# Kernel optimization log

Hardware: AMD Instinct MI355X
Metric: run time of the kernel (lower is better)

Reference implementation:

```python
import jax, jax.numpy as jnp
import numpy as np

B, S, D, H = 16, 4096, 768, 12  # batch, seqlen, dim, num_heads
KS = 9  # res_kernel_size


def setup_inputs() -> dict:
    key = jax.random.key(0)
    ks = jax.random.split(key, 6)
    x = jax.random.normal(ks[0], (B, S, D), dtype=jnp.float32)
    w_qkv = jax.random.normal(ks[1], (3 * D, D), dtype=jnp.float32) * 0.02
    b_qkv = jax.random.normal(ks[2], (3 * D,), dtype=jnp.float32) * 0.02
    w_proj = jax.random.normal(ks[3], (D, D), dtype=jnp.float32) * 0.02
    b_proj = jax.random.normal(ks[4], (D,), dtype=jnp.float32) * 0.02
    # depthwise conv over (seq, head_dim) spatial dims: kernel (KS, 1), groups=H
    w_dconv = jax.random.normal(ks[5], (H, 1, KS, 1), dtype=jnp.float32) * 0.1
    return {"x": x, "w_qkv": w_qkv, "b_qkv": b_qkv,
            "w_proj": w_proj, "b_proj": b_proj, "w_dconv": w_dconv}


def reference(x, w_qkv, b_qkv, w_proj, b_proj, w_dconv):
    Bz, Sz, Dz = x.shape
    Hh = w_dconv.shape[0]
    d = Dz // Hh  # head_dim
    # qkv projection: [B,S,3D] -> [3,B,H,S,d]  (rearrange 's (n h d) -> n h s d')
    qkv = jnp.einsum('bsd,ed->bse', x, w_qkv) + b_qkv
    qkv = qkv.reshape(Bz, Sz, 3, Hh, d).transpose(2, 0, 3, 1, 4)
    q, k, v = qkv[0], qkv[1], qkv[2]  # each [B,H,S,d]
    # L2-normalize q, k along head dim
    q = q / jnp.linalg.norm(q, axis=-1, keepdims=True)
    k = k / jnp.linalg.norm(k, axis=-1, keepdims=True)
    # depthwise conv on v: NCHW = [B, H, S, d], kernel (KS,1), pad (KS//2, 0)
    pad = w_dconv.shape[2] // 2
    dconv_v = jax.lax.conv_general_dilated(
        v, w_dconv, window_strides=(1, 1),
        padding=((pad, pad), (0, 0)), feature_group_count=Hh)
    # linear angular attention: kv = k^T v  ([B,H,d,d]), then q @ kv
    kv = jnp.einsum('bhsd,bhse->bhde', k, v)
    out = 0.5 * v + (1.0 / jnp.pi) * jnp.einsum('bhsd,bhde->bhse', q, kv)
    out = out / jnp.linalg.norm(out, axis=-1, keepdims=True)
    out = out + dconv_v
    # 'h s d -> s (h d)' (with batch): [B,H,S,d] -> [B,S,H*d]
    out = out.transpose(0, 2, 1, 3).reshape(Bz, Sz, Dz)
    return jnp.einsum('bsd,ed->bse', out, w_proj) + b_proj
```

## Files before the change

### kernel.cpp

```cpp
#include <hip/hip_runtime.h>
#include <hip/hip_bf16.h>

#define DEV __device__ __forceinline__

typedef __attribute__((ext_vector_type(8))) short bf16x8;
typedef __attribute__((ext_vector_type(4))) float f32x4;

DEV unsigned short bfbits(float x) {
    __hip_bfloat16 b = __float2bfloat16(x);
    return __builtin_bit_cast(unsigned short, b);
}
DEV float b2f(unsigned short u) {
    __hip_bfloat16 b = __builtin_bit_cast(__hip_bfloat16, u);
    return __bfloat162float(b);
}

DEV void gl2lds16(const void* g, void* l) {
    __builtin_amdgcn_global_load_lds(
        (const __attribute__((address_space(1))) void*)g,
        (__attribute__((address_space(3))) void*)l,
        16, 0, 0);
}

DEV void stC(float* p, float v) { *p = v; }
DEV void stC(__hip_bfloat16* p, float v) { *p = __float2bfloat16(v); }

__global__ __launch_bounds__(256) void cvt_bf16(const float* __restrict__ in,
                                                unsigned short* __restrict__ out, int n) {
    int i = (blockIdx.x * 256 + threadIdx.x) * 4;
    if (i >= n) return;
    float4 f = *(const float4*)(in + i);
    ushort4 u;
    u.x = bfbits(f.x); u.y = bfbits(f.y); u.z = bfbits(f.z); u.w = bfbits(f.w);
    *(ushort4*)(out + i) = u;
}

template <typename OutT>
__global__ __launch_bounds__(256) void gemm_bt(const __hip_bfloat16* __restrict__ A,
                                               const __hip_bfloat16* __restrict__ B,
                                               const float* __restrict__ bias,
                                               OutT* __restrict__ C,
                                               int M, int N, int K) {
    __shared__ __align__(16) unsigned short As[128 * 32];
    __shared__ __align__(16) unsigned short Bs[128 * 32];
    const int t = threadIdx.x;
    const int wave = t >> 6, lane = t & 63;
    const int quad = lane >> 4, l16 = lane & 15;
    const int m0 = blockIdx.y * 128, n0 = blockIdx.x * 128;
    const int wm = (wave & 1) * 64, wn = (wave >> 1) * 64;
    const int r0 = t >> 2;
    const int c0 = (t & 3) * 8;
    const unsigned short* Au = (const unsigned short*)A;
    const unsigned short* Bu = (const unsigned short*)B;

    f32x4 acc[4][4] = {};
    for (int k0 = 0; k0 < K; k0 += 32) {
        gl2lds16(Au + (size_t)(m0 + r0) * K + k0 + c0,      As + t * 8);
        gl2lds16(Au + (size_t)(m0 + 64 + r0) * K + k0 + c0, As + 2048 + t * 8);
        gl2lds16(Bu + (size_t)(n0 + r0) * K + k0 + c0,      Bs + t * 8);
        gl2lds16(Bu + (size_t)(n0 + 64 + r0) * K + k0 + c0, Bs + 2048 + t * 8);
        __syncthreads();
        bf16x8 af[4], bfr[4];
#pragma unroll
        for (int i = 0; i < 4; i++)
            af[i] = *(const bf16x8*)&As[(wm + i * 16 + l16) * 32 + quad * 8];
#pragma unroll
        for (int j = 0; j < 4; j++)
            bfr[j] = *(const bf16x8*)&Bs[(wn + j * 16 + l16) * 32 + quad * 8];
#pragma unroll
        for (int i = 0; i < 4; i++)
#pragma unroll
            for (int j = 0; j < 4; j++)
                acc[i][j] = __builtin_amdgcn_mfma_f32_16x16x32_bf16(af[i], bfr[j], acc[i][j], 0, 0, 0);
        __syncthreads();
    }
#pragma unroll
    for (int i = 0; i < 4; i++) {
#pragma unroll
        for (int j = 0; j < 4; j++) {
            int col = n0 + wn + j * 16 + l16;
            float bv = bias[col];
#pragma unroll
            for (int r = 0; r < 4; r++) {
                int row = m0 + wm + i * 16 + quad * 4 + r;
                stC(C + (size_t)row * N + col, acc[i][j][r] + bv);
            }
        }
    }
}

__global__ __launch_bounds__(256) void gemm_qkv(const __hip_bfloat16* __restrict__ A,
                                                const __hip_bfloat16* __restrict__ B,
                                                const float* __restrict__ bias,
                                                unsigned short* __restrict__ qhat,
                                                unsigned short* __restrict__ khat,
                                                unsigned short* __restrict__ varr) {
    const int K = 768, NN = 2304;
    __shared__ __align__(16) unsigned short As[128 * 32];
    __shared__ __align__(16) unsigned short Bs[128 * 32];
    const int t = threadIdx.x;
    const int wave = t >> 6, lane = t & 63;
    const int quad = lane >> 4, l16 = lane & 15;
    const int m0 = blockIdx.y * 128, n0 = blockIdx.x * 128;
    const int wm = (wave & 1) * 64, wn = (wave >> 1) * 64;
    const int r0 = t >> 2;
    const int c0 = (t & 3) * 8;
    const unsigned short* Au = (const unsigned short*)A;
    const unsigned short* Bu = (const unsigned short*)B;

    f32x4 acc[4][4] = {};
    for (int k0 = 0; k0 < K; k0 += 32) {
        gl2lds16(Au + (size_t)(m0 + r0) * K + k0 + c0,      As + t * 8);
        gl2lds16(Au + (size_t)(m0 + 64 + r0) * K + k0 + c0, As + 2048 + t * 8);
        gl2lds16(Bu + (size_t)(n0 + r0) * K + k0 + c0,      Bs + t * 8);
        gl2lds16(Bu + (size_t)(n0 + 64 + r0) * K + k0 + c0, Bs + 2048 + t * 8);
        __syncthreads();
        bf16x8 af[4], bfr[4];
#pragma unroll
        for (int i = 0; i < 4; i++)
            af[i] = *(const bf16x8*)&As[(wm + i * 16 + l16) * 32 + quad * 8];
#pragma unroll
        for (int j = 0; j < 4; j++)
            bfr[j] = *(const bf16x8*)&Bs[(wn + j * 16 + l16) * 32 + quad * 8];
#pragma unroll
        for (int i = 0; i < 4; i++)
#pragma unroll
            for (int j = 0; j < 4; j++)
                acc[i][j] = __builtin_amdgcn_mfma_f32_16x16x32_bf16(af[i], bfr[j], acc[i][j], 0, 0, 0);
        __syncthreads();
    }

    const int colbase = n0 + wn;
    const int sec = colbase / 768;
    const int cin = colbase - sec * 768;
    const int h = cin >> 6;
    const int b = m0 >> 12;
    unsigned short* dst = (sec == 0) ? qhat : (sec == 1) ? khat : varr;
    float bv[4];
#pragma unroll
    for (int j = 0; j < 4; j++) bv[j] = bias[colbase + j * 16 + l16];

    const size_t headbase = (size_t)(b * 12 + h) * 4096;
#pragma unroll
    for (int i = 0; i < 4; i++) {
        float o[4][4];
#pragma unroll
        for (int j = 0; j < 4; j++)
#pragma unroll
            for (int r = 0; r < 4; r++) o[j][r] = acc[i][j][r] + bv[j];
        if (sec < 2) {
#pragma unroll
            for (int r = 0; r < 4; r++) {
                float ss = o[0][r]*o[0][r] + o[1][r]*o[1][r] + o[2][r]*o[2][r] + o[3][r]*o[3][r];
                ss += __shfl_xor(ss, 1, 64);
                ss += __shfl_xor(ss, 2, 64);
                ss += __shfl_xor(ss, 4, 64);
                ss += __shfl_xor(ss, 8, 64);
                float sc = rsqrtf(ss);
#pragma unroll
                for (int j = 0; j < 4; j++) o[j][r] *= sc;
            }
        }
#pragma unroll
        for (int j = 0; j < 4; j++)
#pragma unroll
            for (int r = 0; r < 4; r++) {
                int s = (m0 + wm + i * 16 + quad * 4 + r) & 4095;
                dst[(headbase + s) * 64 + j * 16 + l16] = bfbits(o[j][r]);
            }
    }
}

__global__ __launch_bounds__(256) void kv_kernel(const unsigned short* __restrict__ khat,
                                                 const unsigned short* __restrict__ varr,
                                                 float* __restrict__ kvpart) {
    const int bh = blockIdx.x >> 2, chunk = blockIdx.x & 3;
    const int t = threadIdx.x, wave = t >> 6, lane = t & 63;
    __shared__ __align__(16) float kt[64 * 64];
    __shared__ __align__(16) float vt[64 * 64];
    const int e0 = (lane >> 3) * 8, f0 = (lane & 7) * 8;
    float acc[8][8] = {};

    for (int tile = 0; tile < 16; tile++) {
        int sbase = chunk * 1024 + tile * 64;
        __syncthreads();
#pragma unroll
        for (int i = 0; i < 2; i++) {
            int c = t + i * 256;
            int row = c >> 3, off = (c & 7) * 8;
            size_t g = ((size_t)bh * 4096 + sbase + row) * 64 + off;
            bf16x8 kk = *(const bf16x8*)(khat + g);
            bf16x8 vv = *(const bf16x8*)(varr + g);
#pragma unroll
            for (int j = 0; j < 8; j++) {
                kt[row * 64 + off + j] = b2f((unsigned short)kk[j]);
                vt[row * 64 + off + j] = b2f((unsigned short)vv[j]);
            }
        }
        __syncthreads();
#pragma unroll
        for (int dsi = 0; dsi < 16; dsi++) {
            int ds = wave * 16 + dsi;
            f32x4 ka = *(f32x4*)&kt[ds * 64 + e0], kb = *(f32x4*)&kt[ds * 64 + e0 + 4];
            f32x4 va = *(f32x4*)&vt[ds * 64 + f0], vb = *(f32x4*)&vt[ds * 64 + f0 + 4];
            float ke[8] = {ka.x, ka.y, ka.z, ka.w, kb.x, kb.y, kb.z, kb.w};
            float vf[8] = {va.x, va.y, va.z, va.w, vb.x, vb.y, vb.z, vb.w};
#pragma unroll
            for (int i = 0; i < 8; i++)
#pragma unroll
                for (int j = 0; j < 8; j++) acc[i][j] += ke[i] * vf[j];
        }
    }
    __syncthreads();
    float* red = kt;
    for (int w = 0; w < 4; w++) {
        if (wave == w) {
#pragma unroll
            for (int i = 0; i < 8; i++)
#pragma unroll
                for (int j = 0; j < 8; j++) {
                    int idx = (e0 + i) * 64 + f0 + j;
                    if (w == 0) red[idx] = acc[i][j];
                    else        red[idx] += acc[i][j];
                }
        }
        __syncthreads();
    }
    float* outp = kvpart + (size_t)blockIdx.x * 4096;
#pragma unroll
    for (int i = 0; i < 16; i++) outp[t + i * 256] = red[t + i * 256];
}

__global__ __launch_bounds__(256) void kvred_kernel(const float* __restrict__ kvpart,
                                                    unsigned short* __restrict__ kvT) {
    const int bh = blockIdx.x;
    const int t = threadIdx.x;
    __shared__ float kvf[64 * 65];
    const float* p0 = kvpart + (size_t)(bh * 4) * 4096;
#pragma unroll
    for (int i = 0; i < 16; i++) {
        int idx = t + i * 256;
        int e = idx >> 6, f = idx & 63;
        kvf[e * 65 + f] = p0[idx] + p0[4096 + idx] + p0[8192 + idx] + p0[12288 + idx];
    }
    __syncthreads();
#pragma unroll
    for (int i = 0; i < 16; i++) {
        int o = t + i * 256;
        int f = o >> 6, e = o & 63;
        kvT[(size_t)bh * 4096 + o] = bfbits(kvf[e * 65 + f]);
    }
}

__global__ __launch_bounds__(256) void attn_kernel(const unsigned short* __restrict__ qhat,
                                                   const unsigned short* __restrict__ varr,
                                                   const unsigned short* __restrict__ kvT,
                                                   const float* __restrict__ wdconv,
                                                   __hip_bfloat16* __restrict__ outpre) {
    const int st = blockIdx.x;
    const int bh = blockIdx.y;
    const int b = bh / 12, h = bh % 12;
    const int s0 = st * 128;
    const int t = threadIdx.x, w = t >> 6, lane = t & 63;
    const int quad = lane >> 4, l16 = lane & 15;

    __shared__ __align__(16) unsigned short vt[136 * 64];
    __shared__ float oL[128 * 65];

    const size_t vb = (size_t)bh * 4096;
#pragma unroll
    for (int i = 0; i < 5; i++) {
        int c = t + i * 256;
        if (c < 1088) {
            int row = c >> 3, off = (c & 7) * 8;
            int gs = s0 - 4 + row;
            bf16x8 vv = {};
            if ((unsigned)gs < 4096u) vv = *(const bf16x8*)(varr + (vb + gs) * 64 + off);
            *(bf16x8*)&vt[row * 64 + off] = vv;
        }
    }

    bf16x8 bfr[2][4];
#pragma unroll
    for (int ks = 0; ks < 2; ks++)
#pragma unroll
        for (int j = 0; j < 4; j++)
            bfr[ks][j] = *(const bf16x8*)(kvT + (size_t)bh * 4096 + (j * 16 + l16) * 64 + ks * 32 + quad * 8);

    f32x4 acc[2][4] = {};
#pragma unroll
    for (int i = 0; i < 2; i++) {
#pragma unroll
        for (int ks = 0; ks < 2; ks++) {
            bf16x8 af = *(const bf16x8*)(qhat + (vb + s0 + w * 32 + i * 16 + l16) * 64 + ks * 32 + quad * 8);
#pragma unroll
            for (int j = 0; j < 4; j++)
                acc[i][j] = __builtin_amdgcn_mfma_f32_16x16x32_bf16(af, bfr[ks][j], acc[i][j], 0, 0, 0);
        }
    }
    __syncthreads();

    const float inv_pi = 0.3183098861837907f;
#pragma unroll
    for (int i = 0; i < 2; i++) {
        float o[4][4];
#pragma unroll
        for (int r = 0; r < 4; r++) {
            int rl = w * 32 + i * 16 + quad * 4 + r;
#pragma unroll
            for (int j = 0; j < 4; j++) {
                float vval = b2f(vt[(rl + 4) * 64 + j * 16 + l16]);
                o[j][r] = 0.5f * vval + inv_pi * acc[i][j][r];
            }
            float ss = o[0][r]*o[0][r] + o[1][r]*o[1][r] + o[2][r]*o[2][r] + o[3][r]*o[3][r];
            ss += __shfl_xor(ss, 1, 64);
            ss += __shfl_xor(ss, 2, 64);
            ss += __shfl_xor(ss, 4, 64);
            ss += __shfl_xor(ss, 8, 64);
            float sc = rsqrtf(ss);
#pragma unroll
            for (int j = 0; j < 4; j++)
                oL[rl * 65 + j * 16 + l16] = o[j][r] * sc;
        }
    }
    __syncthreads();

    float wc[9];
#pragma unroll
    for (int j = 0; j < 9; j++) wc[j] = wdconv[h * 9 + j];
#pragma unroll
    for (int i = 0; i < 32; i++) {
        int c = t + i * 256;
        int sl = c >> 6, f = c & 63;
        float cc = 0.f;
#pragma unroll
        for (int j = 0; j < 9; j++) cc += wc[j] * b2f(vt[(sl + j) * 64 + f]);
        float oo = oL[sl * 65 + f] + cc;
        outpre[(size_t)(b * 4096 + s0 + sl) * 768 + h * 64 + f] = __float2bfloat16(oo);
    }
}

extern "C" void kernel_launch(void* const* d_in, const int* in_sizes, int n_in,
                              void* d_out, int out_size, void* d_ws, size_t ws_size,
                              hipStream_t stream) {
    const float* x      = (const float*)d_in[0];
    const float* w_qkv  = (const float*)d_in[1];
    const float* b_qkv  = (const float*)d_in[2];
    const float* w_proj = (const float*)d_in[3];
    const float* b_proj = (const float*)d_in[4];
    const float* w_dc   = (const float*)d_in[5];
    float* out = (float*)d_out;

    char* ws = (char*)d_ws;
    __hip_bfloat16* xb      = (__hip_bfloat16*)(ws + 0);
    __hip_bfloat16* wqkvb   = (__hip_bfloat16*)(ws + 100663296);
    __hip_bfloat16* wprojb  = (__hip_bfloat16*)(ws + 104202240);
    unsigned short* qhat    = (unsigned short*)(ws + 105381888);
    unsigned short* khat    = (unsigned short*)(ws + 206045184);
    unsigned short* varr    = (unsigned short*)(ws + 306708480);
    float* kvpart           = (float*)(ws + 407371776);
    unsigned short* kvT     = (unsigned short*)(ws + 419954688);
    __hip_bfloat16* outpreb = xb;

    const int NX = 16 * 4096 * 768;
    const int NWQ = 2304 * 768;
    const int NWP = 768 * 768;

    cvt_bf16<<<NX / 1024, 256, 0, stream>>>(x, (unsigned short*)xb, NX);
    cvt_bf16<<<NWQ / 1024, 256, 0, stream>>>(w_qkv, (unsigned short*)wqkvb, NWQ);
    cvt_bf16<<<NWP / 1024, 256, 0, stream>>>(w_proj, (unsigned short*)wprojb, NWP);

    gemm_qkv<<<dim3(2304 / 128, 65536 / 128), 256, 0, stream>>>(
        xb, wqkvb, b_qkv, qhat, khat, varr);

    kv_kernel<<<192 * 4, 256, 0, stream>>>(khat, varr, kvpart);

    kvred_kernel<<<192, 256, 0, stream>>>(kvpart, kvT);

    attn_kernel<<<dim3(32, 192), 256, 0, stream>>>(qhat, varr, kvT, w_dc, (__hip_bfloat16*)xb);

    gemm_bt<float><<<dim3(768 / 128, 65536 / 128), 256, 0, stream>>>(
        (__hip_bfloat16*)xb, wprojb, b_proj, out, 65536, 768, 768);
}
```

Before: 981.8 us.

## Replace GEMMs with 256x256 double-buffered pipelined MFMA kernel with swizzled LDS

Replaces the two 128x128 single-buffered GEMM kernels with one templated 256x256-tile, 512-thread kernel. It double-buffers LDS with asynchronous global-to-LDS loads, waits on vmcnt and uses raw barriers, XOR-swizzles LDS columns to avoid bank conflicts, remaps workgroups in a grouped order and raises wave priority around MFMA blocks. The QKV normalisation epilogue and the plain bias epilogue are kept as template variants. The goal is to overlap memory loads with MFMA and cut the barrier stalls per K step. In exchange it uses 128KB of LDS and more accumulator registers per thread, which may limit occupancy.

New measurement: 877.4 us. -10.6%, faster.

```diff
diff --git a/kernel.cpp b/kernel.cpp
--- a/kernel.cpp
+++ b/kernel.cpp
@@ -22,8 +22,9 @@
         16, 0, 0);
 }
 
-DEV void stC(float* p, float v) { *p = v; }
-DEV void stC(__hip_bfloat16* p, float v) { *p = __float2bfloat16(v); }
+#define WAIT_VM4()  asm volatile("s_waitcnt vmcnt(4)" ::: "memory")
+#define WAIT_VM0()  asm volatile("s_waitcnt vmcnt(0)" ::: "memory")
+#define BARRIER()   asm volatile("s_barrier"          ::: "memory")
 
 __global__ __launch_bounds__(256) void cvt_bf16(const float* __restrict__ in,
                                                 unsigned short* __restrict__ out, int n) {
@@ -35,139 +36,164 @@
     *(ushort4*)(out + i) = u;
 }
 
-template <typename OutT>
-__global__ __launch_bounds__(256) void gemm_bt(const __hip_bfloat16* __restrict__ A,
-                                               const __hip_bfloat16* __restrict__ B,
-                                               const float* __restrict__ bias,
-                                               OutT* __restrict__ C,
-                                               int M, int N, int K) {
-    __shared__ __align__(16) unsigned short As[128 * 32];
-    __shared__ __align__(16) unsigned short Bs[128 * 32];
+template <int EPI>
+__global__ __launch_bounds__(512, 2) void gemm256(
+        const unsigned short* __restrict__ A,
+        const unsigned short* __restrict__ B,
+        const float* __restrict__ bias,
+        float* __restrict__ Cf,
+        unsigned short* __restrict__ qhat,
+        unsigned short* __restrict__ khat,
+        unsigned short* __restrict__ varr,
+        int N) {
+    constexpr int K = 768, NT = 12;
+    __shared__ __align__(16) unsigned short sh[65536];
     const int t = threadIdx.x;
     const int wave = t >> 6, lane = t & 63;
     const int quad = lane >> 4, l16 = lane & 15;
-    const int m0 = blockIdx.y * 128, n0 = blockIdx.x * 128;
-    const int wm = (wave & 1) * 64, wn = (wave >> 1) * 64;
-    const int r0 = t >> 2;
-    const int c0 = (t & 3) * 8;
-    const unsigned short* Au = (const unsigned short*)A;
-    const unsigned short* Bu = (const unsigned short*)B;
-
-    f32x4 acc[4][4] = {};
-    for (int k0 = 0; k0 < K; k0 += 32) {
-        gl2lds16(Au + (size_t)(m0 + r0) * K + k0 + c0,      As + t * 8);
-        gl2lds16(Au + (size_t)(m0 + 64 + r0) * K + k0 + c0, As + 2048 + t * 8);
-        gl2lds16(Bu + (size_t)(n0 + r0) * K + k0 + c0,      Bs + t * 8);
-        gl2lds16(Bu + (size_t)(n0 + 64 + r0) * K + k0 + c0, Bs + 2048 + t * 8);
-        __syncthreads();
-        bf16x8 af[4], bfr[4];
+    const int wm = wave >> 2, wn = wave & 3;
+
+    const int gx = gridDim.x;
+    const int nwg = gx * gridDim.y;
+    const int wg0 = blockIdx.y * gx + blockIdx.x;
+    const int swz = (wg0 & 7) * (nwg >> 3) + (wg0 >> 3);
+    const int m0 = (swz / gx) * 256;
+    const int n0 = (swz % gx) * 256;
+
+    const unsigned short* Abase = A + (size_t)m0 * K;
+    const unsigned short* Bbase = B + (size_t)n0 * K;
+
+    const int scb = (t & 3) ^ ((t >> 3) & 3);
+    const size_t soff = (size_t)(t >> 2) * K + scb * 8;
+    auto STAGE = [&](const unsigned short* g, unsigned short* l) {
+        gl2lds16(g + soff, l + t * 8);
+        gl2lds16(g + soff + 128 * K, l + 4096 + t * 8);
+    };
+
+    const int cb8 = (quad ^ ((l16 >> 1) & 3)) * 8;
+    const int aoff = (wm * 128 + l16) * 32 + cb8;
+    const int boff = (wn * 64 + l16) * 32 + cb8;
+
+    STAGE(Abase,      sh);
+    STAGE(Bbase,      sh + 16384);
+    STAGE(Abase + 32, sh + 8192);
+    STAGE(Bbase + 32, sh + 24576);
+
+    f32x4 acc[8][4] = {};
+
+#pragma unroll 2
+    for (int kt = 0; kt < NT; ++kt) {
+        unsigned short* buf  = sh + (kt & 1) * 32768;
+        unsigned short* nbuf = sh + ((kt + 1) & 1) * 32768;
+        const unsigned short* An = Abase + (kt + 1) * 64;
+        const unsigned short* Bn = Bbase + (kt + 1) * 64;
+        bf16x8 afr[4], bfr[4];
+
+        WAIT_VM4();
+        BARRIER();
+#pragma unroll
+        for (int i = 0; i < 4; i++) afr[i] = *(const bf16x8*)(buf + aoff + i * 512);
+#pragma unroll
+        for (int j = 0; j < 4; j++) bfr[j] = *(const bf16x8*)(buf + 16384 + boff + j * 512);
+        if (kt + 1 < NT) STAGE(An, nbuf);
+        __builtin_amdgcn_s_setprio(1);
 #pragma unroll
         for (int i = 0; i < 4; i++)
-            af[i] = *(const bf16x8*)&As[(wm + i * 16 + l16) * 32 + quad * 8];
-#pragma unroll
-        for (int j = 0; j < 4; j++)
-            bfr[j] = *(const bf16x8*)&Bs[(wn + j * 16 + l16) * 32 + quad * 8];
+#pragma unroll
+            for (int j = 0; j < 4; j++)
+                acc[i][j] = __builtin_amdgcn_mfma_f32_16x16x32_bf16(afr[i], bfr[j], acc[i][j], 0, 0, 0);
+        __builtin_amdgcn_s_setprio(0);
+
+#pragma unroll
+        for (int i = 0; i < 4; i++) afr[i] = *(const bf16x8*)(buf + aoff + (i + 4) * 512);
+        if (kt + 1 < NT) STAGE(Bn, nbuf + 16384);
+        __builtin_amdgcn_s_setprio(1);
 #pragma unroll
         for (int i = 0; i < 4; i++)
 #pragma unroll
             for (int j = 0; j < 4; j++)
-                acc[i][j] = __builtin_amdgcn_mfma_f32_16x16x32_bf16(af[i], bfr[j], acc[i][j], 0, 0, 0);
-        __syncthreads();
-    }
-#pragma unroll
-    for (int i = 0; i < 4; i++) {
+                acc[i + 4][j] = __builtin_amdgcn_mfma_f32_16x16x32_bf16(afr[i], bfr[j], acc[i + 4][j], 0, 0, 0);
+        __builtin_amdgcn_s_setprio(0);
+
+        if (kt + 1 < NT) { WAIT_VM4(); } else { WAIT_VM0(); }
+        BARRIER();
+#pragma unroll
+        for (int i = 0; i < 4; i++) afr[i] = *(const bf16x8*)(buf + 8192 + aoff + i * 512);
+#pragma unroll
+        for (int j = 0; j < 4; j++) bfr[j] = *(const bf16x8*)(buf + 24576 + boff + j * 512);
+        if (kt + 1 < NT) STAGE(An + 32, nbuf + 8192);
+        __builtin_amdgcn_s_setprio(1);
+#pragma unroll
+        for (int i = 0; i < 4; i++)
+#pragma unroll
+            for (int j = 0; j < 4; j++)
+                acc[i][j] = __builtin_amdgcn_mfma_f32_16x16x32_bf16(afr[i], bfr[j], acc[i][j], 0, 0, 0);
+        __builtin_amdgcn_s_setprio(0);
+
+#pragma unroll
+        for (int i = 0; i < 4; i++) afr[i] = *(const bf16x8*)(buf + 8192 + aoff + (i + 4) * 512);
+        if (kt + 1 < NT) STAGE(Bn + 32, nbuf + 24576);
+        __builtin_amdgcn_s_setprio(1);
+#pragma unroll
+        for (int i = 0; i < 4; i++)
+#pragma unroll
+            for (int j = 0; j < 4; j++)
+                acc[i + 4][j] = __builtin_amdgcn_mfma_f32_16x16x32_bf16(afr[i], bfr[j], acc[i + 4][j], 0, 0, 0);
+        __builtin_amdgcn_s_setprio(0);
+    }
+
+    const int colbase = n0 + wn * 64;
+    if constexpr (EPI == 0) {
 #pragma unroll
         for (int j = 0; j < 4; j++) {
-            int col = n0 + wn + j * 16 + l16;
+            int col = colbase + j * 16 + l16;
             float bv = bias[col];
 #pragma unroll
-            for (int r = 0; r < 4; r++) {
-                int row = m0 + wm + i * 16 + quad * 4 + r;
-                stC(C + (size_t)row * N + col, acc[i][j][r] + bv);
+            for (int i = 0; i < 8; i++)
+#pragma unroll
+                for (int r = 0; r < 4; r++) {
+                    int row = m0 + wm * 128 + i * 16 + quad * 4 + r;
+                    Cf[(size_t)row * N + col] = acc[i][j][r] + bv;
+                }
+        }
+    } else {
+        const int sec = colbase / 768;
+        const int cin = colbase - sec * 768;
+        const int h = cin >> 6;
+        const int b = m0 >> 12;
+        unsigned short* dst = (sec == 0) ? qhat : (sec == 1) ? khat : varr;
+        const size_t headbase = (size_t)(b * 12 + h) * 4096;
+        float bv[4];
+#pragma unroll
+        for (int j = 0; j < 4; j++) bv[j] = bias[colbase + j * 16 + l16];
+#pragma unroll
+        for (int i = 0; i < 8; i++) {
+            float o[4][4];
+#pragma unroll
+            for (int j = 0; j < 4; j++)
+#pragma unroll
+                for (int r = 0; r < 4; r++) o[j][r] = acc[i][j][r] + bv[j];
+            if (sec < 2) {
+#pragma unroll
+                for (int r = 0; r < 4; r++) {
+                    float ss = o[0][r]*o[0][r] + o[1][r]*o[1][r] + o[2][r]*o[2][r] + o[3][r]*o[3][r];
+                    ss += __shfl_xor(ss, 1, 64);
+                    ss += __shfl_xor(ss, 2, 64);
+                    ss += __shfl_xor(ss, 4, 64);
+                    ss += __shfl_xor(ss, 8, 64);
+                    float sc = rsqrtf(ss);
+#pragma unroll
+                    for (int j = 0; j < 4; j++) o[j][r] *= sc;
+                }
             }
-        }
-    }
-}
-
-__global__ __launch_bounds__(256) void gemm_qkv(const __hip_bfloat16* __restrict__ A,
-                                                const __hip_bfloat16* __restrict__ B,
-                                                const float* __restrict__ bias,
-                                                unsigned short* __restrict__ qhat,
-                                                unsigned short* __restrict__ khat,
-                                                unsigned short* __restrict__ varr) {
-    const int K = 768, NN = 2304;
-    __shared__ __align__(16) unsigned short As[128 * 32];
-    __shared__ __align__(16) unsigned short Bs[128 * 32];
-    const int t = threadIdx.x;
-    const int wave = t >> 6, lane = t & 63;
-    const int quad = lane >> 4, l16 = lane & 15;
-    const int m0 = blockIdx.y * 128, n0 = blockIdx.x * 128;
-    const int wm = (wave & 1) * 64, wn = (wave >> 1) * 64;
-    const int r0 = t >> 2;
-    const int c0 = (t & 3) * 8;
-    const unsigned short* Au = (const unsigned short*)A;
-    const unsigned short* Bu = (const unsigned short*)B;
-
-    f32x4 acc[4][4] = {};
-    for (int k0 = 0; k0 < K; k0 += 32) {
-        gl2lds16(Au + (size_t)(m0 + r0) * K + k0 + c0,      As + t * 8);
-        gl2lds16(Au + (size_t)(m0 + 64 + r0) * K + k0 + c0, As + 2048 + t * 8);
-        gl2lds16(Bu + (size_t)(n0 + r0) * K + k0 + c0,      Bs + t * 8);
-        gl2lds16(Bu + (size_t)(n0 + 64 + r0) * K + k0 + c0, Bs + 2048 + t * 8);
-        __syncthreads();
-        bf16x8 af[4], bfr[4];
-#pragma unroll
-        for (int i = 0; i < 4; i++)
-            af[i] = *(const bf16x8*)&As[(wm + i * 16 + l16) * 32 + quad * 8];
-#pragma unroll
-        for (int j = 0; j < 4; j++)
-            bfr[j] = *(const bf16x8*)&Bs[(wn + j * 16 + l16) * 32 + quad * 8];
-#pragma unroll
-        for (int i = 0; i < 4; i++)
-#pragma unroll
-            for (int j = 0; j < 4; j++)
-                acc[i][j] = __builtin_amdgcn_mfma_f32_16x16x32_bf16(af[i], bfr[j], acc[i][j], 0, 0, 0);
-        __syncthreads();
-    }
-
-    const int colbase = n0 + wn;
-    const int sec = colbase / 768;
-    const int cin = colbase - sec * 768;
-    const int h = cin >> 6;
-    const int b = m0 >> 12;
-    unsigned short* dst = (sec == 0) ? qhat : (sec == 1) ? khat : varr;
-    float bv[4];
-#pragma unroll
-    for (int j = 0; j < 4; j++) bv[j] = bias[colbase + j * 16 + l16];
-
-    const size_t headbase = (size_t)(b * 12 + h) * 4096;
-#pragma unroll
-    for (int i = 0; i < 4; i++) {
-        float o[4][4];
-#pragma unroll
-        for (int j = 0; j < 4; j++)
-#pragma unroll
-            for (int r = 0; r < 4; r++) o[j][r] = acc[i][j][r] + bv[j];
-        if (sec < 2) {
-#pragma unroll
-            for (int r = 0; r < 4; r++) {
-                float ss = o[0][r]*o[0][r] + o[1][r]*o[1][r] + o[2][r]*o[2][r] + o[3][r]*o[3][r];
-                ss += __shfl_xor(ss, 1, 64);
-                ss += __shfl_xor(ss, 2, 64);
-                ss += __shfl_xor(ss, 4, 64);
-                ss += __shfl_xor(ss, 8, 64);
-                float sc = rsqrtf(ss);
-#pragma unroll
-                for (int j = 0; j < 4; j++) o[j][r] *= sc;
-            }
-        }
-#pragma unroll
-        for (int j = 0; j < 4; j++)
-#pragma unroll
-            for (int r = 0; r < 4; r++) {
-                int s = (m0 + wm + i * 16 + quad * 4 + r) & 4095;
-                dst[(headbase + s) * 64 + j * 16 + l16] = bfbits(o[j][r]);
-            }
+#pragma unroll
+            for (int j = 0; j < 4; j++)
+#pragma unroll
+                for (int r = 0; r < 4; r++) {
+                    int s = (m0 + wm * 128 + i * 16 + quad * 4 + r) & 4095;
+                    dst[(headbase + s) * 64 + j * 16 + l16] = bfbits(o[j][r]);
+                }
+        }
     }
 }
 
@@ -352,26 +378,25 @@
     float* out = (float*)d_out;
 
     char* ws = (char*)d_ws;
-    __hip_bfloat16* xb      = (__hip_bfloat16*)(ws + 0);
-    __hip_bfloat16* wqkvb   = (__hip_bfloat16*)(ws + 100663296);
-    __hip_bfloat16* wprojb  = (__hip_bfloat16*)(ws + 104202240);
+    unsigned short* xb      = (unsigned short*)(ws + 0);
+    unsigned short* wqkvb   = (unsigned short*)(ws + 100663296);
+    unsigned short* wprojb  = (unsigned short*)(ws + 104202240);
     unsigned short* qhat    = (unsigned short*)(ws + 105381888);
     unsigned short* khat    = (unsigned short*)(ws + 206045184);
     unsigned short* varr    = (unsigned short*)(ws + 306708480);
     float* kvpart           = (float*)(ws + 407371776);
     unsigned short* kvT     = (unsigned short*)(ws + 419954688);
-    __hip_bfloat16* outpreb = xb;
 
     const int NX = 16 * 4096 * 768;
     const int NWQ = 2304 * 768;
     const int NWP = 768 * 768;
 
-    cvt_bf16<<<NX / 1024, 256, 0, stream>>>(x, (unsigned short*)xb, NX);
-    cvt_bf16<<<NWQ / 1024, 256, 0, stream>>>(w_qkv, (unsigned short*)wqkvb, NWQ);
-    cvt_bf16<<<NWP / 1024, 256, 0, stream>>>(w_proj, (unsigned short*)wprojb, NWP);
-
-    gemm_qkv<<<dim3(2304 / 128, 65536 / 128), 256, 0, stream>>>(
-        xb, wqkvb, b_qkv, qhat, khat, varr);
+    cvt_bf16<<<NX / 1024, 256, 0, stream>>>(x, xb, NX);
+    cvt_bf16<<<NWQ / 1024, 256, 0, stream>>>(w_qkv, wqkvb, NWQ);
+    cvt_bf16<<<NWP / 1024, 256, 0, stream>>>(w_proj, wprojb, NWP);
+
+    gemm256<1><<<dim3(2304 / 256, 65536 / 256), 512, 0, stream>>>(
+        xb, wqkvb, b_qkv, nullptr, qhat, khat, varr, 2304);
 
     kv_kernel<<<192 * 4, 256, 0, stream>>>(khat, varr, kvpart);
 
@@ -379,6 +404,6 @@
 
     attn_kernel<<<dim3(32, 192), 256, 0, stream>>>(qhat, varr, kvT, w_dc, (__hip_bfloat16*)xb);
 
-    gemm_bt<float><<<dim3(768 / 128, 65536 / 128), 256, 0, stream>>>(
-        (__hip_bfloat16*)xb, wprojb, b_proj, out, 65536, 768, 768);
-}
+    gemm256<0><<<dim3(768 / 256, 65536 / 256), 512, 0, stream>>>(
+        xb, wprojb, b_proj, out, nullptr, nullptr, nullptr, 768);
+}
```
